# Optimization experiments

Measured on AMD Instinct MI355X. Metric: run time of the kernel, lower is better.

Reference implementation:

```python
import jax, jax.numpy as jnp
import numpy as np
import itertools

FS, C_SOUND, NMICS, NTDOAS, MAX_TAU, TRACKS = 24000, 343, 4, 6, 6, 5
B, T, TR, NCLS = 64, 500, 5, 13
NLOGIT = 2 * MAX_TAU + 1  # 13 TDOA classes
IGNORE = -100
_PAIRS = np.array([(m1, m2) for m1 in range(NMICS) for m2 in range(m1 + 1, NMICS)])  # [6,2]
_PERMS = np.array(list(itertools.permutations(range(TRACKS))))  # [120,5]


def _mic_locs():
    coords = [[0.042, 45, 35], [0.042, -45, -35], [0.042, 135, -35], [0.042, -135, 35]]
    locs = []
    for rad, azi, ele in coords:
        azi, ele = np.deg2rad(azi), np.deg2rad(ele)
        locs.append([rad * np.cos(azi) * np.cos(ele), rad * np.sin(azi) * np.cos(ele), rad * np.sin(ele)])
    return np.array(locs, dtype=np.float32)


def setup_inputs() -> dict:
    key = jax.random.key(0)
    k1, k2, k3, k4 = jax.random.split(key, 4)
    pred = jax.random.normal(k1, (B, T, NLOGIT, TR, NTDOAS), dtype=jnp.float32)
    active = (jax.random.uniform(k2, (B, T, TR, NCLS)) < 0.06).astype(jnp.float32)
    doa = jax.random.normal(k3, (B, T, TR, 3, NCLS), dtype=jnp.float32)
    doa = doa / jnp.linalg.norm(doa, axis=3, keepdims=True)
    dist = jax.random.uniform(k4, (B, T, TR, NCLS), minval=1.0, maxval=5.0, dtype=jnp.float32)
    target = jnp.concatenate([active[:, :, :, None, :], doa, dist[:, :, :, None, :]], axis=3)
    return {"pred": pred, "target": target, "mic_locs": jnp.asarray(_mic_locs())}


def _tdoa_targets(target, mic_locs):
    # target: [B,T,Tr,5,C] -> int32 class targets [B,T,Tr,NTDOAS]
    Bs, Ts, Tr, _, C = target.shape
    active = target[:, :, :, 0, :] != 0                                   # [B,T,Tr,C]
    src = jnp.moveaxis(target[:, :, :, 1:4, :] * target[:, :, :, 4:5, :], 3, -1)  # [B,T,Tr,C,3]
    d = jnp.linalg.norm(src[..., None, :] - mic_locs[None, None, None, None], axis=-1)  # [B,T,Tr,C,4]
    tdoa = d[..., _PAIRS[:, 0]] - d[..., _PAIRS[:, 1]]                    # [B,T,Tr,C,6]
    cls = jnp.round(tdoa * FS / C_SOUND).astype(jnp.int32) + MAX_TAU      # in [0, 2*max_tau]
    # pack first Tr active sources (tr-major, class-minor order) into track slots
    act_flat = active.reshape(Bs, Ts, Tr * C)
    cls_flat = cls.reshape(Bs, Ts, Tr * C, NTDOAS)
    order = jnp.argsort(jnp.logical_not(act_flat).astype(jnp.int32), axis=-1, stable=True)
    sel = order[:, :, :Tr]                                                # [B,T,Tr]
    vals = jnp.take_along_axis(cls_flat, sel[..., None], axis=2)          # [B,T,Tr,6]
    slot_ok = jnp.arange(Tr)[None, None, :] < act_flat.sum(-1)[..., None]
    return jnp.where(slot_ok[..., None], vals, IGNORE)


def reference(pred, target, mic_locs):
    tdoas = _tdoa_targets(target, mic_locs)                               # [B,T,Tr,P]
    Bs, Ts, CL, Tr, P = pred.shape
    N = Bs * Ts * P
    tgt = jnp.transpose(tdoas, (0, 1, 3, 2)).reshape(N, Tr)               # [N,Tr]
    logits = jnp.transpose(pred, (0, 1, 4, 2, 3)).reshape(N, CL, Tr)      # [N,CL,Tr]
    logp = jax.nn.log_softmax(logits, axis=1)
    valid = tgt != IGNORE
    safe = jnp.where(valid, tgt, 0)
    idx = jnp.broadcast_to(safe[:, :, None], (N, Tr, Tr))
    ce = jnp.take_along_axis(logp, idx, axis=1)                           # ce[n,i,j] = logp[n, tgt[n,i], j]
    loss_mat = jnp.where(valid[:, :, None], -ce, 0.0)                     # ignore_index -> 0 loss
    cost = loss_mat[:, np.arange(Tr)[None, :], _PERMS].mean(-1)           # [N,120]
    loss = cost.min(axis=1).mean()
    best = jnp.take(jnp.asarray(_PERMS), cost.argmin(axis=1), axis=0)     # [N,Tr]
    pred_cls = logits.argmax(axis=1)                                      # [N,Tr]
    tgt_perm = jnp.take_along_axis(tgt, best, axis=1)
    vp = tgt_perm != IGNORE
    n_pred = vp.sum()
    correct = ((pred_cls == tgt_perm) & vp).sum()
    acc = jnp.where(n_pred > 0, correct / jnp.maximum(n_pred, 1), 0.0).astype(jnp.float32)
    return loss, acc
```

## Files before the change

kernel.cpp:

```cpp
#include <hip/hip_runtime.h>
#include <hip/hip_bf16.h>
#include <math.h>

#define NCELLS 32000
#define NP_ 6
#define IGN (-100)
#define CPB 64
#define NBLK (NCELLS / CPB)
#define THREADS 384

struct PermTable { int p[120][5]; };
constexpr PermTable make_perms() {
    PermTable t{};
    for (int i = 0; i < 120; ++i) {
        int avail[5] = {0, 1, 2, 3, 4};
        int rem = i;
        const int f[5] = {24, 6, 2, 1, 1};
        for (int k = 0; k < 5; ++k) {
            int d = rem / f[k];
            rem = rem % f[k];
            t.p[i][k] = avail[d];
            for (int m = d; m < 4 - k; ++m) avail[m] = avail[m + 1];
        }
    }
    return t;
}
__device__ constexpr PermTable PT = make_perms();

__global__ __launch_bounds__(THREADS) void tdoa_fused(
        const float* __restrict__ pred, const float* __restrict__ target,
        const float* __restrict__ mic,
        float* __restrict__ costp, int* __restrict__ vpp, int* __restrict__ crp) {
    __shared__ int cnt[CPB][5];
    __shared__ int scls[CPB][NP_][5];
    const int j = threadIdx.x;
    const int blk = blockIdx.x;

    if (j < CPB * 5) {
        const int cellL = j / 5, tr = j - cellL * 5;
        const int cell = blk * CPB + cellL;
        const float* __restrict__ tg = target + (size_t)cell * 325 + tr * 65;

        float fl[13];
#pragma unroll
        for (int c = 0; c < 13; ++c) fl[c] = tg[c];
        int mycnt = 0;
#pragma unroll
        for (int c = 0; c < 13; ++c) mycnt += (fl[c] != 0.0f) ? 1 : 0;
        cnt[cellL][tr] = mycnt;
        __syncthreads();

        int base = 0, total = 0;
#pragma unroll
        for (int t = 0; t < 5; ++t) {
            int v = cnt[cellL][t];
            total += v;
            if (t < tr) base += v;
        }

        if (tr == 0) {
            for (int s = (total < 5 ? total : 5); s < 5; ++s)
#pragma unroll
                for (int p = 0; p < 6; ++p) scls[cellL][p][s] = IGN;
        }

        float mx[4], my[4], mz[4];
#pragma unroll
        for (int m = 0; m < 4; ++m) {
            mx[m] = mic[m * 3 + 0];
            my[m] = mic[m * 3 + 1];
            mz[m] = mic[m * 3 + 2];
        }

        int slot = base;
#pragma unroll
        for (int c = 0; c < 13; ++c) {
            if (fl[c] != 0.0f) {
                if (slot < 5) {
                    float dist = tg[52 + c];
                    float sx = tg[13 + c] * dist;
                    float sy = tg[26 + c] * dist;
                    float sz = tg[39 + c] * dist;
                    float d[4];
#pragma unroll
                    for (int m = 0; m < 4; ++m) {
                        float dx = sx - mx[m], dy = sy - my[m], dz = sz - mz[m];
                        d[m] = sqrtf(dx * dx + dy * dy + dz * dz);
                    }
                    const int Q0[6] = {0, 0, 0, 1, 1, 2};
                    const int Q1[6] = {1, 2, 3, 2, 3, 3};
#pragma unroll
                    for (int q = 0; q < 6; ++q) {
                        float td = (d[Q0[q]] - d[Q1[q]]) * (24000.0f / 343.0f);
                        int cls = (int)rintf(td) + 6;
                        cls = cls < 0 ? 0 : (cls > 12 ? 12 : cls);
                        scls[cellL][q][slot] = cls;
                    }
                }
                ++slot;
            }
        }
    } else {
        __syncthreads();
    }
    __syncthreads();

    const int cellL = j / NP_, p = j - cellL * NP_;
    const float* __restrict__ L =
        pred + (size_t)(blk * CPB + cellL) * 390 + p;

    float lse[5];
    int amax[5];
#pragma unroll
    for (int tr = 0; tr < 5; ++tr) {
        float v[13];
#pragma unroll
        for (int c = 0; c < 13; ++c) v[c] = L[c * 30 + tr * 6];
        float m = v[0];
        int am = 0;
#pragma unroll
        for (int c = 1; c < 13; ++c) {
            if (v[c] > m) { m = v[c]; am = c; }
        }
        float s = 0.0f;
#pragma unroll
        for (int c = 0; c < 13; ++c) s += __expf(v[c] - m);
        lse[tr] = m + __logf(s);
        amax[tr] = am;
    }

    int tcs[5];
#pragma unroll
    for (int slot = 0; slot < 5; ++slot) tcs[slot] = scls[cellL][p][slot];

    float lm[5][5];
#pragma unroll
    for (int slot = 0; slot < 5; ++slot) {
        bool val = (tcs[slot] != IGN);
        int tcc = val ? tcs[slot] : 0;
        tcc = min(max(tcc, 0), 12);
#pragma unroll
        for (int tr = 0; tr < 5; ++tr) {
            float g = L[tcc * 30 + tr * 6];
            lm[slot][tr] = val ? (lse[tr] - g) : 0.0f;
        }
    }

    float best = 1e30f;
    int bi = 0;
#pragma unroll
    for (int i = 0; i < 120; ++i) {
        float c = lm[0][PT.p[i][0]] + lm[1][PT.p[i][1]] + lm[2][PT.p[i][2]]
                + lm[3][PT.p[i][3]] + lm[4][PT.p[i][4]];
        if (c < best) { best = c; bi = i; }
    }
    float mycost = best * (1.0f / 5.0f);

    int vp = 0, cr = 0;
#pragma unroll
    for (int k = 0; k < 5; ++k) {
        int slot = PT.p[bi][k];
        int tc = tcs[slot];
        if (tc != IGN) {
            ++vp;
            if (amax[k] == tc) ++cr;
        }
    }

    float rc = mycost;
    int rv = vp, rr = cr;
#pragma unroll
    for (int off = 32; off > 0; off >>= 1) {
        rc += __shfl_down(rc, off, 64);
        rv += __shfl_down(rv, off, 64);
        rr += __shfl_down(rr, off, 64);
    }
    __shared__ float sf[6];
    __shared__ int sv[6], sc2[6];
    const int wave = j >> 6, lane = j & 63;
    if (lane == 0) { sf[wave] = rc; sv[wave] = rv; sc2[wave] = rr; }
    __syncthreads();
    if (j == 0) {
        float c = 0.0f;
        int v = 0, r = 0;
#pragma unroll
        for (int w = 0; w < 6; ++w) { c += sf[w]; v += sv[w]; r += sc2[w]; }
        costp[blk] = c;
        vpp[blk] = v;
        crp[blk] = r;
    }
}

__global__ __launch_bounds__(256) void tdoa_final(
        const float* __restrict__ costp, const int* __restrict__ vpp,
        const int* __restrict__ crp, float* __restrict__ out) {
    __shared__ float sf[4];
    __shared__ int sv[4], sc[4];
    int j = threadIdx.x;
    float c = 0.0f;
    int v = 0, r = 0;
    for (int i = j; i < NBLK; i += 256) {
        c += costp[i];
        v += vpp[i];
        r += crp[i];
    }
#pragma unroll
    for (int off = 32; off > 0; off >>= 1) {
        c += __shfl_down(c, off, 64);
        v += __shfl_down(v, off, 64);
        r += __shfl_down(r, off, 64);
    }
    int wave = j >> 6, lane = j & 63;
    if (lane == 0) { sf[wave] = c; sv[wave] = v; sc[wave] = r; }
    __syncthreads();
    if (j == 0) {
        float tc = sf[0] + sf[1] + sf[2] + sf[3];
        int tv = sv[0] + sv[1] + sv[2] + sv[3];
        int trr = sc[0] + sc[1] + sc[2] + sc[3];
        out[0] = tc / (float)(NCELLS * NP_);
        out[1] = (tv > 0) ? ((float)trr / (float)tv) : 0.0f;
    }
}

extern "C" void kernel_launch(void* const* d_in, const int* in_sizes, int n_in,
                              void* d_out, int out_size, void* d_ws, size_t ws_size,
                              hipStream_t stream) {
    const float* pred   = (const float*)d_in[0];
    const float* target = (const float*)d_in[1];
    const float* mic    = (const float*)d_in[2];
    float* out = (float*)d_out;

    float* costp = (float*)d_ws;
    int*   vpp   = (int*)((char*)d_ws + NBLK * 4);
    int*   crp   = (int*)((char*)d_ws + NBLK * 8);

    tdoa_fused<<<NBLK, THREADS, 0, stream>>>(pred, target, mic, costp, vpp, crp);
    tdoa_final<<<1, 256, 0, stream>>>(costp, vpp, crp, out);
}
```

Baseline: 135.5 us.

## Split per-track softmax across lanes and shrink blocks to eight cells

Each (cell, pair) group now uses five lanes, one per track, to compute log-sum-exp and argmax. The 5x5 cost matrix is assembled with wave shuffles before each lane runs the 120-permutation search redundantly. Blocks shrink to 8 cells and 256 threads, giving many more blocks and more parallelism per cell. The cost is four idle lanes per wave, the shuffle traffic, and duplicated permutation search across the five lanes.

```diff
diff --git a/kernel.cpp b/kernel.cpp
--- a/kernel.cpp
+++ b/kernel.cpp
@@ -5,9 +5,9 @@
 #define NCELLS 32000
 #define NP_ 6
 #define IGN (-100)
-#define CPB 64
+#define CPB 8
 #define NBLK (NCELLS / CPB)
-#define THREADS 384
+#define THREADS 256
 
 struct PermTable { int p[120][5]; };
 constexpr PermTable make_perms() {
@@ -36,34 +36,32 @@
     const int j = threadIdx.x;
     const int blk = blockIdx.x;
 
+    float fl[13];
+    const int cellS = j / 5, trS = j - cellS * 5;
+    const float* __restrict__ tg =
+        target + (size_t)(blk * CPB + (cellS < CPB ? cellS : 0)) * 325 + trS * 65;
     if (j < CPB * 5) {
-        const int cellL = j / 5, tr = j - cellL * 5;
-        const int cell = blk * CPB + cellL;
-        const float* __restrict__ tg = target + (size_t)cell * 325 + tr * 65;
-
-        float fl[13];
 #pragma unroll
         for (int c = 0; c < 13; ++c) fl[c] = tg[c];
         int mycnt = 0;
 #pragma unroll
         for (int c = 0; c < 13; ++c) mycnt += (fl[c] != 0.0f) ? 1 : 0;
-        cnt[cellL][tr] = mycnt;
-        __syncthreads();
-
+        cnt[cellS][trS] = mycnt;
+    }
+    __syncthreads();
+    if (j < CPB * 5) {
         int base = 0, total = 0;
 #pragma unroll
         for (int t = 0; t < 5; ++t) {
-            int v = cnt[cellL][t];
+            int v = cnt[cellS][t];
             total += v;
-            if (t < tr) base += v;
-        }
-
-        if (tr == 0) {
+            if (t < trS) base += v;
+        }
+        if (trS == 0) {
             for (int s = (total < 5 ? total : 5); s < 5; ++s)
 #pragma unroll
-                for (int p = 0; p < 6; ++p) scls[cellL][p][s] = IGN;
-        }
-
+                for (int p = 0; p < 6; ++p) scls[cellS][p][s] = IGN;
+        }
         float mx[4], my[4], mz[4];
 #pragma unroll
         for (int m = 0; m < 4; ++m) {
@@ -71,7 +69,6 @@
             my[m] = mic[m * 3 + 1];
             mz[m] = mic[m * 3 + 2];
         }
-
         int slot = base;
 #pragma unroll
         for (int c = 0; c < 13; ++c) {
@@ -94,25 +91,25 @@
                         float td = (d[Q0[q]] - d[Q1[q]]) * (24000.0f / 343.0f);
                         int cls = (int)rintf(td) + 6;
                         cls = cls < 0 ? 0 : (cls > 12 ? 12 : cls);
-                        scls[cellL][q][slot] = cls;
+                        scls[cellS][q][slot] = cls;
                     }
                 }
                 ++slot;
             }
         }
-    } else {
-        __syncthreads();
-    }
-    __syncthreads();
-
-    const int cellL = j / NP_, p = j - cellL * NP_;
-    const float* __restrict__ L =
-        pred + (size_t)(blk * CPB + cellL) * 390 + p;
-
-    float lse[5];
-    int amax[5];
-#pragma unroll
-    for (int tr = 0; tr < 5; ++tr) {
+    }
+    __syncthreads();
+
+    const int wave = j >> 6, lane = j & 63;
+    float rc = 0.0f;
+    int rv = 0, rr = 0;
+    if (lane < 60) {
+        const int grp = lane / 5, tr = lane - grp * 5;
+        const int g = wave * 12 + grp;
+        const int cellL = g / NP_, p = g - cellL * NP_;
+        const float* __restrict__ L =
+            pred + (size_t)(blk * CPB + cellL) * 390 + p;
+
         float v[13];
 #pragma unroll
         for (int c = 0; c < 13; ++c) v[c] = L[c * 30 + tr * 6];
@@ -125,69 +122,59 @@
         float s = 0.0f;
 #pragma unroll
         for (int c = 0; c < 13; ++c) s += __expf(v[c] - m);
-        lse[tr] = m + __logf(s);
-        amax[tr] = am;
-    }
-
-    int tcs[5];
-#pragma unroll
-    for (int slot = 0; slot < 5; ++slot) tcs[slot] = scls[cellL][p][slot];
-
-    float lm[5][5];
-#pragma unroll
-    for (int slot = 0; slot < 5; ++slot) {
-        bool val = (tcs[slot] != IGN);
-        int tcc = val ? tcs[slot] : 0;
-        tcc = min(max(tcc, 0), 12);
-#pragma unroll
-        for (int tr = 0; tr < 5; ++tr) {
-            float g = L[tcc * 30 + tr * 6];
-            lm[slot][tr] = val ? (lse[tr] - g) : 0.0f;
-        }
-    }
-
-    float best = 1e30f;
-    int bi = 0;
-#pragma unroll
-    for (int i = 0; i < 120; ++i) {
-        float c = lm[0][PT.p[i][0]] + lm[1][PT.p[i][1]] + lm[2][PT.p[i][2]]
-                + lm[3][PT.p[i][3]] + lm[4][PT.p[i][4]];
-        if (c < best) { best = c; bi = i; }
-    }
-    float mycost = best * (1.0f / 5.0f);
-
-    int vp = 0, cr = 0;
-#pragma unroll
-    for (int k = 0; k < 5; ++k) {
-        int slot = PT.p[bi][k];
-        int tc = tcs[slot];
+        const float lse = m + __logf(s);
+
+        float lmc[5];
+#pragma unroll
+        for (int slot = 0; slot < 5; ++slot) {
+            int tcs = scls[cellL][p][slot];
+            bool val = (tcs != IGN);
+            int tcc = val ? tcs : 0;
+            float gl = L[tcc * 30 + tr * 6];
+            lmc[slot] = val ? (lse - gl) : 0.0f;
+        }
+
+        const int gb5 = grp * 5;
+        float lmf[5][5];
+#pragma unroll
+        for (int slot = 0; slot < 5; ++slot)
+#pragma unroll
+            for (int t = 0; t < 5; ++t)
+                lmf[slot][t] = __shfl(lmc[slot], gb5 + t, 64);
+
+        float best = 1e30f;
+        int bi = 0;
+#pragma unroll
+        for (int i = 0; i < 120; ++i) {
+            float c = lmf[0][PT.p[i][0]] + lmf[1][PT.p[i][1]]
+                    + lmf[2][PT.p[i][2]] + lmf[3][PT.p[i][3]]
+                    + lmf[4][PT.p[i][4]];
+            if (c < best) { best = c; bi = i; }
+        }
+        if (tr == 0) rc = best * (1.0f / 5.0f);
+
+        int slot = PT.p[bi][tr];
+        int tc = scls[cellL][p][slot];
         if (tc != IGN) {
-            ++vp;
-            if (amax[k] == tc) ++cr;
-        }
-    }
-
-    float rc = mycost;
-    int rv = vp, rr = cr;
+            rv = 1;
+            rr = (am == tc) ? 1 : 0;
+        }
+    }
+
 #pragma unroll
     for (int off = 32; off > 0; off >>= 1) {
         rc += __shfl_down(rc, off, 64);
         rv += __shfl_down(rv, off, 64);
         rr += __shfl_down(rr, off, 64);
     }
-    __shared__ float sf[6];
-    __shared__ int sv[6], sc2[6];
-    const int wave = j >> 6, lane = j & 63;
+    __shared__ float sf[4];
+    __shared__ int sv[4], sc2[4];
     if (lane == 0) { sf[wave] = rc; sv[wave] = rv; sc2[wave] = rr; }
     __syncthreads();
     if (j == 0) {
-        float c = 0.0f;
-        int v = 0, r = 0;
-#pragma unroll
-        for (int w = 0; w < 6; ++w) { c += sf[w]; v += sv[w]; r += sc2[w]; }
-        costp[blk] = c;
-        vpp[blk] = v;
-        crp[blk] = r;
+        costp[blk] = sf[0] + sf[1] + sf[2] + sf[3];
+        vpp[blk]   = sv[0] + sv[1] + sv[2] + sv[3];
+        crp[blk]   = sc2[0] + sc2[1] + sc2[2] + sc2[3];
     }
 }
 
```

Result: slower. 148.0 us (+9.2%).
